# Kernel optimization log

Measured on AMD Instinct MI355X. Metric: run time of the kernel, lower is better.

Reference implementation:

```python
import jax, jax.numpy as jnp
import numpy as np

B, S, H, NH = 2, 2048, 1024, 16
P = H // NH

def setup_inputs() -> dict:
    key = jax.random.key(0)
    k1, k2, k3, k4 = jax.random.split(key, 4)
    x = jax.random.normal(k1, (B, S, H), dtype=jnp.float32)
    mask = jax.random.randint(k2, (B, S), 0, 2).astype(jnp.int32)
    # weights: (num_heads, 3, hidden, partial) -- the leading singleton dim of the
    # torch parameter is pure broadcast, dropped here.
    W = jax.random.normal(k3, (NH, 3, H, P), dtype=jnp.float32) * (1.0 / np.sqrt(H))
    Wl = jax.random.normal(k4, (H, H), dtype=jnp.float32) * (1.0 / np.sqrt(H))
    bl = jnp.zeros((H,), dtype=jnp.float32)
    return {"x": x, "mask": mask, "W": W, "Wl": Wl, "bl": bl}

def reference(x, mask, W, Wl, bl):
    nh, _, h, p = W.shape
    scale = 1.0 / np.sqrt(p)
    # kvq[b, t, n, s, p]; t=0 keys, t=1 values, t=2 queries (unbind order in source)
    kvq = jnp.einsum('bsh,nthp->btnsp', x, W)
    keys, values, queries = kvq[:, 0], kvq[:, 1], kvq[:, 2]  # each [B, NH, S, P]
    # NOTE: source computes keys @ queries^T -> scores[b,n,i,j] = k_i . q_j
    scores = jnp.einsum('bnip,bnjp->bnij', keys, queries) * scale
    # mask==0 zeroes out the LAST axis (query positions), exactly as the fancy-index write
    scores = jnp.where(mask[:, None, None, :] == 0, jnp.float32(-1e12), scores)
    # softmax over dim=2 (key axis), as in the source (Softmax(dim=2))
    w = jax.nn.softmax(scores, axis=2)
    out = jnp.einsum('bnij,bnjp->bnip', w, values)  # [B, NH, S, P]
    b, _, s, _ = out.shape
    hidden = out.transpose(0, 2, 1, 3).reshape(b, s, nh * p)  # concat heads
    return hidden @ Wl.T + bl
```

## Files before the change

### kernel.cpp

```cpp
#include <hip/hip_runtime.h>

#define B_ 2
#define S_ 2048
#define H_ 1024
#define NH_ 16
#define P_ 64

using f32x4 = __attribute__((ext_vector_type(4))) float;
using i32x4 = __attribute__((ext_vector_type(4))) int;
using f16   = _Float16;
using f16x8 = __attribute__((ext_vector_type(8))) f16;
using f16x4 = __attribute__((ext_vector_type(4))) f16;
using h16x2 = __attribute__((ext_vector_type(2))) __fp16;

#define QSCALE 0.18033688f

static __device__ __forceinline__ f16x8 ldh8(const f16* p) { return *(const f16x8*)p; }
static __device__ __forceinline__ f32x4 ld4f(const float* p) { return *(const f32x4*)p; }

static __device__ __forceinline__ f32x4 mm16(f16x8 a, f16x8 b, f32x4 c) {
  return __builtin_amdgcn_mfma_f32_16x16x32_f16(a, b, c, 0, 0, 0);
}

__global__ __launch_bounds__(256) void tw_kernel(
    const float* __restrict__ W, f16* __restrict__ WtH)
{
  __shared__ float T[64 * 65];
  const int tid = threadIdx.x;
  const int nt = blockIdx.x >> 4;
  const int h0 = (blockIdx.x & 15) * 64;
  const float* src = W + (size_t)nt * H_ * P_ + (size_t)h0 * P_;
  #pragma unroll
  for (int r = 0; r < 4; ++r) {
    int idx = tid + r * 256;
    int h = idx >> 4, p4 = (idx & 15) << 2;
    f32x4 v = ld4f(src + (size_t)h * P_ + p4);
    #pragma unroll
    for (int i = 0; i < 4; ++i) T[(p4 + i) * 65 + h] = v[i];
  }
  __syncthreads();
  f16* dh = WtH + (size_t)nt * P_ * H_;
  #pragma unroll
  for (int r = 0; r < 4; ++r) {
    int idx = tid + r * 256;
    int p = idx >> 4, h4 = (idx & 15) << 2;
    f16x4 hv;
    #pragma unroll
    for (int i = 0; i < 4; ++i) hv[i] = (f16)T[p * 65 + h4 + i];
    *(f16x4*)(dh + (size_t)p * H_ + h0 + h4) = hv;
  }
}

__global__ __launch_bounds__(256) void swl_kernel(
    const float* __restrict__ Wl, f16* __restrict__ WlH)
{
  int idx = blockIdx.x * 256 + threadIdx.x;
  f32x4 v = ((const f32x4*)Wl)[idx];
  f16x4 h;
  #pragma unroll
  for (int i = 0; i < 4; ++i) h[i] = (f16)v[i];
  ((f16x4*)WlH)[idx] = h;
}

__global__ __launch_bounds__(256) void qkv_kernel(
    const float* __restrict__ x, const f16* __restrict__ WtH,
    f16* __restrict__ Kh, f16* __restrict__ Qh, f16* __restrict__ VTh)
{
  __shared__ f16 xls[2][64 * 64];

  int blk = blockIdx.x;
  const int st = blk & 31; blk >>= 5;
  const int n = blk & 15;
  const int b = blk >> 4;
  const int s0 = st * 64;
  const int tid = threadIdx.x;
  const int w = tid >> 6, lane = tid & 63, q = lane >> 4, fr = lane & 15;
  const int bn = b * NH_ + n;

  const int srow = tid >> 2, scc = tid & 3;
  const float* xsrc = x + ((size_t)b * S_ + s0 + srow) * H_ + 16 * scc;
  const int c0 = ((2 * scc) ^ (srow & 7)) * 8;
  const int c1 = ((2 * scc + 1) ^ (srow & 7)) * 8;

  auto stage = [&](int k0, int bs) {
    f32x4 v0 = ld4f(xsrc + k0),     v1 = ld4f(xsrc + k0 + 4);
    f32x4 v2 = ld4f(xsrc + k0 + 8), v3 = ld4f(xsrc + k0 + 12);
    f16x8 a, b2;
    #pragma unroll
    for (int e = 0; e < 4; ++e) {
      a[e] = (f16)v0[e];  a[e + 4] = (f16)v1[e];
      b2[e] = (f16)v2[e]; b2[e + 4] = (f16)v3[e];
    }
    *(f16x8*)&xls[bs][srow * 64 + c0] = a;
    *(f16x8*)&xls[bs][srow * 64 + c1] = b2;
  };

  const f16* WtK = WtH + ((size_t)(n * 3 + 0) * P_ + 16 * w + fr) * H_ + 8 * q;
  const f16* WtV = WtH + ((size_t)(n * 3 + 1) * P_ + 16 * w + fr) * H_ + 8 * q;
  const f16* WtQ = WtH + ((size_t)(n * 3 + 2) * P_ + 16 * w + fr) * H_ + 8 * q;

  f32x4 accK[4] = {}, accQ[4] = {}, accV[4] = {};

  stage(0, 0);
  for (int step = 0; step < 16; ++step) {
    __syncthreads();
    if (step < 15) stage((step + 1) * 64, (step + 1) & 1);
    const int bs = step & 1;
    const int k0 = step * 64;

    f16x8 xf[4][2];
    #pragma unroll
    for (int ss = 0; ss < 4; ++ss) {
      int row = 16 * ss + fr;
      #pragma unroll
      for (int ks = 0; ks < 2; ++ks) {
        int ch = ((q + 4 * ks) ^ (row & 7)) * 8;
        xf[ss][ks] = *(const f16x8*)&xls[bs][row * 64 + ch];
      }
    }
    f16x8 wk0 = ldh8(WtK + k0), wk1 = ldh8(WtK + k0 + 32);
    f16x8 wq0 = ldh8(WtQ + k0), wq1 = ldh8(WtQ + k0 + 32);
    f16x8 wv0 = ldh8(WtV + k0), wv1 = ldh8(WtV + k0 + 32);
    #pragma unroll
    for (int ss = 0; ss < 4; ++ss) {
      accK[ss] = mm16(wk0, xf[ss][0], accK[ss]);
      accK[ss] = mm16(wk1, xf[ss][1], accK[ss]);
      accQ[ss] = mm16(wq0, xf[ss][0], accQ[ss]);
      accQ[ss] = mm16(wq1, xf[ss][1], accQ[ss]);
      accV[ss] = mm16(xf[ss][0], wv0, accV[ss]);
      accV[ss] = mm16(xf[ss][1], wv1, accV[ss]);
    }
  }

  #pragma unroll
  for (int ss = 0; ss < 4; ++ss) {
    f16x4 hK, hQ;
    #pragma unroll
    for (int c = 0; c < 4; ++c) {
      hK[c] = (f16)accK[ss][c];
      hQ[c] = (f16)(accQ[ss][c] * QSCALE);
    }
    size_t off = ((size_t)bn * S_ + (s0 + 16 * ss + fr)) * P_ + 16 * w + 4 * q;
    *(f16x4*)(Kh + off) = hK;
    *(f16x4*)(Qh + off) = hQ;
  }
  #pragma unroll
  for (int ss = 0; ss < 4; ++ss) {
    f16x4 hV;
    #pragma unroll
    for (int c = 0; c < 4; ++c) hV[c] = (f16)accV[ss][c];
    size_t off = ((size_t)bn * P_ + (16 * w + fr)) * S_ + s0 + 16 * ss + 4 * q;
    *(f16x4*)(VTh + off) = hV;
  }
}

__global__ __launch_bounds__(256) void stats_kernel(
    const f16* __restrict__ Kh, const f16* __restrict__ Qh,
    float* __restrict__ csuminv)
{
  __shared__ float zbuf[2 * 128];
  const int tid = threadIdx.x;
  const int bid = blockIdx.x;
  const int j0 = (bid & 15) * 128;
  const int bn = bid >> 4;
  const int w = tid >> 6, lane = tid & 63, q = lane >> 4, fr = lane & 15;
  const int jb = 64 * (w & 1), ih = w >> 1, ib0 = 32 * ih;

  f16x8 qf[4][2];
  #pragma unroll
  for (int jt = 0; jt < 4; ++jt)
    #pragma unroll
    for (int ks = 0; ks < 2; ++ks)
      qf[jt][ks] = ldh8(Qh + ((size_t)bn * S_ + (j0 + jb + 16 * jt + fr)) * P_ + 8 * q + 32 * ks);

  f32x4 z[4] = {};
  f16x8 kA[2][2], kB[2][2];

  auto loadK = [&](f16x8 (&kf)[2][2], int i0) {
    #pragma unroll
    for (int it = 0; it < 2; ++it)
      #pragma unroll
      for (int ks = 0; ks < 2; ++ks)
        kf[it][ks] = ldh8(Kh + ((size_t)bn * S_ + (i0 + ib0 + 16 * it + fr)) * P_ + 8 * q + 32 * ks);
  };
  auto step = [&](f16x8 (&kf)[2][2]) {
    f32x4 sc[4][2] = {};
    __builtin_amdgcn_s_setprio(1);
    #pragma unroll
    for (int ks = 0; ks < 2; ++ks)
      #pragma unroll
      for (int jt = 0; jt < 4; ++jt)
        #pragma unroll
        for (int it = 0; it < 2; ++it)
          sc[jt][it] = mm16(qf[jt][ks], kf[it][ks], sc[jt][it]);
    __builtin_amdgcn_s_setprio(0);
    #pragma unroll
    for (int jt = 0; jt < 4; ++jt)
      #pragma unroll
      for (int c = 0; c < 4; ++c)
        z[jt][c] += exp2f(sc[jt][0][c]) + exp2f(sc[jt][1][c]);
  };

  loadK(kA, 0);
  for (int i0 = 0; i0 < S_; i0 += 128) {
    loadK(kB, i0 + 64);
    step(kA);
    loadK(kA, (i0 + 128) & (S_ - 1));
    step(kB);
  }

  #pragma unroll
  for (int msk = 1; msk <= 8; msk <<= 1)
    #pragma unroll
    for (int jt = 0; jt < 4; ++jt)
      #pragma unroll
      for (int c = 0; c < 4; ++c)
        z[jt][c] += __shfl_xor(z[jt][c], msk, 64);

  if (fr == 0) {
    #pragma unroll
    for (int jt = 0; jt < 4; ++jt)
      *(f32x4*)&zbuf[ih * 128 + jb + 16 * jt + 4 * q] = z[jt];
  }
  __syncthreads();
  if (tid < 128)
    csuminv[(size_t)bn * S_ + j0 + tid] = 1.0f / (zbuf[tid] + zbuf[128 + tid]);
}

__global__ __launch_bounds__(256) void scale_kernel(
    f16* __restrict__ VT, const float* __restrict__ csuminv,
    const int* __restrict__ mask, float* __restrict__ Cbuf)
{
  const int bid = blockIdx.x;
  const int bn = bid >> 4;
  const int b = bn >> 4;
  const int p = (bid & 15) * 4 + (threadIdx.x >> 6);
  const int lane = threadIdx.x & 63;
  f16* row = VT + ((size_t)bn * P_ + p) * S_;
  const float* zr = csuminv + (size_t)bn * S_;
  const int* mr = mask + (size_t)b * S_;
  float acc = 0.0f;
  #pragma unroll
  for (int k = 0; k < 4; ++k) {
    int s = (lane + 64 * k) * 8;
    f16x8 v = *(const f16x8*)(row + s);
    f32x4 z0 = ld4f(zr + s), z1 = ld4f(zr + s + 4);
    i32x4 m0 = *(const i32x4*)(mr + s), m1 = *(const i32x4*)(mr + s + 4);
    f16x8 o;
    #pragma unroll
    for (int e = 0; e < 4; ++e) {
      float fv = (float)v[e];
      if (m0[e] != 0) o[e] = (f16)(fv * z0[e]);
      else { o[e] = (f16)0.0f; acc += fv; }
      float fv2 = (float)v[e + 4];
      if (m1[e] != 0) o[e + 4] = (f16)(fv2 * z1[e]);
      else { o[e + 4] = (f16)0.0f; acc += fv2; }
    }
    *(f16x8*)(row + s) = o;
  }
  #pragma unroll
  for (int msk = 1; msk <= 32; msk <<= 1) acc += __shfl_xor(acc, msk, 64);
  if (lane == 0) Cbuf[bn * P_ + p] = acc * (1.0f / S_);
}

__global__ __launch_bounds__(256) void av_kernel(
    const f16* __restrict__ Kh, const f16* __restrict__ Qh,
    const f16* __restrict__ VT, const float* __restrict__ Cbuf,
    f16* __restrict__ hidh)
{
  __shared__ __align__(16) char smem[18432];
  const int tid = threadIdx.x;
  const int bid = blockIdx.x;
  const int i0 = (bid & 31) * 64;
  const int bn = bid >> 5;
  const int b = bn >> 4, n = bn & 15;
  const int w = tid >> 6, lane = tid & 63, q = lane >> 4, fr = lane & 15;
  f16* ew = (f16*)smem + w * (64 * 36);

  f16x8 kf[4][2];
  #pragma unroll
  for (int it = 0; it < 4; ++it)
    #pragma unroll
    for (int ks = 0; ks < 2; ++ks)
      kf[it][ks] = ldh8(Kh + ((size_t)bn * S_ + (i0 + 16 * it + fr)) * P_ + 8 * q + 32 * ks);

  const f16* qp  = Qh + ((size_t)bn * S_ + (w * 32 + fr)) * P_ + 8 * q;
  const f16* vp0 = VT + ((size_t)bn * P_ + fr) * S_ + w * 32 + 8 * q;
  const f16* vp1 = vp0 + (size_t)16 * S_;
  const f16* vp2 = vp0 + (size_t)32 * S_;
  const f16* vp3 = vp0 + (size_t)48 * S_;

  f32x4 opv[4][4] = {};

  for (int T = 0; T < 16; ++T) {
    f16x8 aq00 = ldh8(qp);
    f16x8 aq01 = ldh8(qp + 32);
    f16x8 aq10 = ldh8(qp + 1024);
    f16x8 aq11 = ldh8(qp + 1056);
    f16x8 va0 = ldh8(vp0), va1 = ldh8(vp1), va2 = ldh8(vp2), va3 = ldh8(vp3);
    qp += 128 * 64;
    vp0 += 128; vp1 += 128; vp2 += 128; vp3 += 128;

    #pragma unroll
    for (int it = 0; it < 4; ++it) {
      f32x4 s0 = {}, s1 = {};
      s0 = mm16(aq00, kf[it][0], s0);
      s0 = mm16(aq01, kf[it][1], s0);
      s1 = mm16(aq10, kf[it][0], s1);
      s1 = mm16(aq11, kf[it][1], s1);
      union { f16x4 v; h16x2 h[2]; } e0, e1;
      e0.h[0] = __builtin_amdgcn_cvt_pkrtz(exp2f(s0[0]), exp2f(s0[1]));
      e0.h[1] = __builtin_amdgcn_cvt_pkrtz(exp2f(s0[2]), exp2f(s0[3]));
      e1.h[0] = __builtin_amdgcn_cvt_pkrtz(exp2f(s1[0]), exp2f(s1[1]));
      e1.h[1] = __builtin_amdgcn_cvt_pkrtz(exp2f(s1[2]), exp2f(s1[3]));
      *(f16x4*)(ew + (16 * it + fr) * 36 + 4 * q)      = e0.v;
      *(f16x4*)(ew + (16 * it + fr) * 36 + 16 + 4 * q) = e1.v;
    }

    #pragma unroll
    for (int it = 0; it < 4; ++it) {
      f16x8 ef = *(const f16x8*)(ew + (16 * it + fr) * 36 + 8 * q);
      opv[0][it] = mm16(va0, ef, opv[0][it]);
      opv[1][it] = mm16(va1, ef, opv[1][it]);
      opv[2][it] = mm16(va2, ef, opv[2][it]);
      opv[3][it] = mm16(va3, ef, opv[3][it]);
    }
  }

  float* accl = (float*)smem;
  #pragma unroll
  for (int r = 0; r < 4; ++r) {
    __syncthreads();
    if (w == r) {
      #pragma unroll
      for (int it = 0; it < 4; ++it)
        #pragma unroll
        for (int pt = 0; pt < 4; ++pt) {
          float* a = &accl[(16 * it + fr) * 68 + 16 * pt + 4 * q];
          if (r == 0) *(f32x4*)a = opv[pt][it];
          else {
            f32x4 old = *(const f32x4*)a;
            #pragma unroll
            for (int c = 0; c < 4; ++c) old[c] += opv[pt][it][c];
            *(f32x4*)a = old;
          }
        }
    }
  }
  __syncthreads();

  const int ti = tid >> 2;
  const int tp = (tid & 3) << 4;
  const float* cb = Cbuf + bn * P_ + tp;
  f16* dst = hidh + ((size_t)b * S_ + (i0 + ti)) * H_ + n * P_ + tp;
  #pragma unroll
  for (int h = 0; h < 2; ++h) {
    f32x4 a0 = *(const f32x4*)&accl[ti * 68 + tp + 8 * h];
    f32x4 a1 = *(const f32x4*)&accl[ti * 68 + tp + 8 * h + 4];
    f32x4 c0 = ld4f(cb + 8 * h);
    f32x4 c1 = ld4f(cb + 8 * h + 4);
    f16x8 o;
    #pragma unroll
    for (int e = 0; e < 4; ++e) {
      o[e]     = (f16)(a0[e] + c0[e]);
      o[e + 4] = (f16)(a1[e] + c1[e]);
    }
    *(f16x8*)(dst + 8 * h) = o;
  }
}

__global__ __launch_bounds__(256) void final_kernel(
    const f16* __restrict__ hidh, const f16* __restrict__ WlH,
    const float* __restrict__ bl, float* __restrict__ out)
{
  __shared__ f16 hl[2][64 * 64];
  const int tid = threadIdx.x;
  const int ot = blockIdx.x & 15;
  const int rt = blockIdx.x >> 4;
  const int r0 = rt * 64, o0 = ot * 64;
  const int w = tid >> 6, lane = tid & 63, q = lane >> 4, fr = lane & 15;

  const int srow = tid >> 2, scc = tid & 3;
  const f16* hsrc = hidh + (size_t)(r0 + srow) * H_ + 16 * scc;
  const int c0 = ((2 * scc) ^ (srow & 7)) * 8;
  const int c1 = ((2 * scc + 1) ^ (srow & 7)) * 8;

  auto stage = [&](int k0, int bs) {
    f16x8 a = ldh8(hsrc + k0);
    f16x8 b2 = ldh8(hsrc + k0 + 8);
    *(f16x8*)&hl[bs][srow * 64 + c0] = a;
    *(f16x8*)&hl[bs][srow * 64 + c1] = b2;
  };

  const f16* WlA = WlH + ((size_t)(o0 + 16 * w + fr)) * H_ + 8 * q;

  f32x4 acc[4] = {};

  stage(0, 0);
  for (int step = 0; step < 16; ++step) {
    __syncthreads();
    if (step < 15) stage((step + 1) * 64, (step + 1) & 1);
    const int bs = step & 1;
    const int k0 = step * 64;

    f16x8 bh[4][2];
    #pragma unroll
    for (int ss = 0; ss < 4; ++ss) {
      int row = 16 * ss + fr;
      #pragma unroll
      for (int ks = 0; ks < 2; ++ks) {
        int ch = ((q + 4 * ks) ^ (row & 7)) * 8;
        bh[ss][ks] = *(const f16x8*)&hl[bs][row * 64 + ch];
      }
    }
    f16x8 ah0 = ldh8(WlA + k0);
    f16x8 ah1 = ldh8(WlA + k0 + 32);
    #pragma unroll
    for (int ss = 0; ss < 4; ++ss) {
      acc[ss] = mm16(ah0, bh[ss][0], acc[ss]);
      acc[ss] = mm16(ah1, bh[ss][1], acc[ss]);
    }
  }

  const int o = o0 + 16 * w + 4 * q;
  f32x4 bv = ld4f(bl + o);
  #pragma unroll
  for (int ss = 0; ss < 4; ++ss) {
    f32x4 v;
    #pragma unroll
    for (int c = 0; c < 4; ++c) v[c] = acc[ss][c] + bv[c];
    *(f32x4*)(out + (size_t)(r0 + 16 * ss + fr) * H_ + o) = v;
  }
}

extern "C" void kernel_launch(void* const* d_in, const int* in_sizes, int n_in,
                              void* d_out, int out_size, void* d_ws, size_t ws_size,
                              hipStream_t stream) {
  const float* x    = (const float*)d_in[0];
  const int*   mask = (const int*)d_in[1];
  const float* W    = (const float*)d_in[2];
  const float* Wl   = (const float*)d_in[3];
  const float* bl   = (const float*)d_in[4];
  float* out = (float*)d_out;

  const size_t SZ  = (size_t)B_ * NH_ * S_ * P_;
  const size_t SZW = (size_t)NH_ * 3 * H_ * P_;
  const size_t SZL = (size_t)H_ * H_;
  const size_t SZC = (size_t)B_ * NH_ * S_;
  const size_t SZH = (size_t)B_ * S_ * H_;

  char* p = (char*)d_ws;
  f16*   Kh   = (f16*)p;  p += SZ * 2;
  f16*   Qh   = (f16*)p;  p += SZ * 2;
  f16*   VTh  = (f16*)p;  p += SZ * 2;
  f16*   WtH  = (f16*)p;  p += SZW * 2;
  f16*   WlH  = (f16*)p;  p += SZL * 2;
  f16*   hidh = (f16*)p;  p += SZH * 2;
  float* csuminv = (float*)p; p += SZC * 4;
  float* Cbuf    = (float*)p; p += (size_t)B_ * NH_ * P_ * 4;

  tw_kernel   <<<NH_ * 3 * (H_ / 64), 256, 0, stream>>>(W, WtH);
  swl_kernel  <<<(SZL / 4) / 256, 256, 0, stream>>>(Wl, WlH);
  qkv_kernel  <<<B_ * NH_ * (S_ / 64), 256, 0, stream>>>(x, WtH, Kh, Qh, VTh);
  stats_kernel<<<B_ * NH_ * (S_ / 128), 256, 0, stream>>>(Kh, Qh, csuminv);
  scale_kernel<<<B_ * NH_ * 16, 256, 0, stream>>>(VTh, csuminv, mask, Cbuf);
  av_kernel   <<<B_ * NH_ * (S_ / 64), 256, 0, stream>>>(
      Kh, Qh, VTh, Cbuf, hidh);
  final_kernel<<<(B_ * S_ / 64) * (H_ / 64), 256, 0, stream>>>(
      hidh, WlH, bl, out);
}
```

Baseline: 218.6 us.

## Fuse weight prep kernels, fold V scaling into stats, keep exp tiles in registers

Merges the two weight-conversion kernels into one launch and folds the V-column scaling and mask-sum into the stats kernel, reducing Cbuf with atomics after a memset. This removes the csuminv round trip and one launch. In the AV kernel, the exponentiated score fragment now feeds the MFMA straight from registers instead of being staged through LDS. To make that valid, V is loaded as two 4-wide halves arranged to match the MFMA operand layout. The costs are float atomic ordering nondeterminism, an extra memset, and narrower V loads.

```diff
diff --git a/kernel.cpp b/kernel.cpp
--- a/kernel.cpp
+++ b/kernel.cpp
@@ -16,50 +16,50 @@
 #define QSCALE 0.18033688f
 
 static __device__ __forceinline__ f16x8 ldh8(const f16* p) { return *(const f16x8*)p; }
+static __device__ __forceinline__ f16x4 ldh4(const f16* p) { return *(const f16x4*)p; }
 static __device__ __forceinline__ f32x4 ld4f(const float* p) { return *(const f32x4*)p; }
 
 static __device__ __forceinline__ f32x4 mm16(f16x8 a, f16x8 b, f32x4 c) {
   return __builtin_amdgcn_mfma_f32_16x16x32_f16(a, b, c, 0, 0, 0);
 }
 
-__global__ __launch_bounds__(256) void tw_kernel(
-    const float* __restrict__ W, f16* __restrict__ WtH)
+__global__ __launch_bounds__(256) void prep_kernel(
+    const float* __restrict__ W, const float* __restrict__ Wl,
+    f16* __restrict__ WtH, f16* __restrict__ WlH)
 {
   __shared__ float T[64 * 65];
   const int tid = threadIdx.x;
-  const int nt = blockIdx.x >> 4;
-  const int h0 = (blockIdx.x & 15) * 64;
-  const float* src = W + (size_t)nt * H_ * P_ + (size_t)h0 * P_;
-  #pragma unroll
-  for (int r = 0; r < 4; ++r) {
-    int idx = tid + r * 256;
-    int h = idx >> 4, p4 = (idx & 15) << 2;
-    f32x4 v = ld4f(src + (size_t)h * P_ + p4);
-    #pragma unroll
-    for (int i = 0; i < 4; ++i) T[(p4 + i) * 65 + h] = v[i];
-  }
-  __syncthreads();
-  f16* dh = WtH + (size_t)nt * P_ * H_;
-  #pragma unroll
-  for (int r = 0; r < 4; ++r) {
-    int idx = tid + r * 256;
-    int p = idx >> 4, h4 = (idx & 15) << 2;
-    f16x4 hv;
-    #pragma unroll
-    for (int i = 0; i < 4; ++i) hv[i] = (f16)T[p * 65 + h4 + i];
-    *(f16x4*)(dh + (size_t)p * H_ + h0 + h4) = hv;
-  }
-}
-
-__global__ __launch_bounds__(256) void swl_kernel(
-    const float* __restrict__ Wl, f16* __restrict__ WlH)
-{
-  int idx = blockIdx.x * 256 + threadIdx.x;
-  f32x4 v = ((const f32x4*)Wl)[idx];
-  f16x4 h;
-  #pragma unroll
-  for (int i = 0; i < 4; ++i) h[i] = (f16)v[i];
-  ((f16x4*)WlH)[idx] = h;
+  if (blockIdx.x < 768) {
+    const int nt = blockIdx.x >> 4;
+    const int h0 = (blockIdx.x & 15) * 64;
+    const float* src = W + (size_t)nt * H_ * P_ + (size_t)h0 * P_;
+    #pragma unroll
+    for (int r = 0; r < 4; ++r) {
+      int idx = tid + r * 256;
+      int h = idx >> 4, p4 = (idx & 15) << 2;
+      f32x4 v = ld4f(src + (size_t)h * P_ + p4);
+      #pragma unroll
+      for (int i = 0; i < 4; ++i) T[(p4 + i) * 65 + h] = v[i];
+    }
+    __syncthreads();
+    f16* dh = WtH + (size_t)nt * P_ * H_;
+    #pragma unroll
+    for (int r = 0; r < 4; ++r) {
+      int idx = tid + r * 256;
+      int p = idx >> 4, h4 = (idx & 15) << 2;
+      f16x4 hv;
+      #pragma unroll
+      for (int i = 0; i < 4; ++i) hv[i] = (f16)T[p * 65 + h4 + i];
+      *(f16x4*)(dh + (size_t)p * H_ + h0 + h4) = hv;
+    }
+  } else {
+    int idx = (blockIdx.x - 768) * 256 + tid;
+    f32x4 v = ((const f32x4*)Wl)[idx];
+    f16x4 h;
+    #pragma unroll
+    for (int i = 0; i < 4; ++i) h[i] = (f16)v[i];
+    ((f16x4*)WlH)[idx] = h;
+  }
 }
 
 __global__ __launch_bounds__(256) void qkv_kernel(
@@ -156,7 +156,8 @@
 
 __global__ __launch_bounds__(256) void stats_kernel(
     const f16* __restrict__ Kh, const f16* __restrict__ Qh,
-    float* __restrict__ csuminv)
+    f16* __restrict__ VT, const int* __restrict__ mask,
+    float* __restrict__ Cbuf)
 {
   __shared__ float zbuf[2 * 128];
   const int tid = threadIdx.x;
@@ -224,43 +225,29 @@
   }
   __syncthreads();
   if (tid < 128)
-    csuminv[(size_t)bn * S_ + j0 + tid] = 1.0f / (zbuf[tid] + zbuf[128 + tid]);
-}
-
-__global__ __launch_bounds__(256) void scale_kernel(
-    f16* __restrict__ VT, const float* __restrict__ csuminv,
-    const int* __restrict__ mask, float* __restrict__ Cbuf)
-{
-  const int bid = blockIdx.x;
-  const int bn = bid >> 4;
-  const int b = bn >> 4;
-  const int p = (bid & 15) * 4 + (threadIdx.x >> 6);
-  const int lane = threadIdx.x & 63;
-  f16* row = VT + ((size_t)bn * P_ + p) * S_;
-  const float* zr = csuminv + (size_t)bn * S_;
-  const int* mr = mask + (size_t)b * S_;
+    zbuf[tid] = 1.0f / (zbuf[tid] + zbuf[128 + tid]);
+  __syncthreads();
+
+  const int sp = tid >> 2;
+  const int jc = (tid & 3) * 32;
+  f16* vrow = VT + ((size_t)bn * P_ + sp) * S_ + j0 + jc;
+  const int* mr = mask + (size_t)(bn >> 4) * S_ + j0 + jc;
   float acc = 0.0f;
   #pragma unroll
   for (int k = 0; k < 4; ++k) {
-    int s = (lane + 64 * k) * 8;
-    f16x8 v = *(const f16x8*)(row + s);
-    f32x4 z0 = ld4f(zr + s), z1 = ld4f(zr + s + 4);
-    i32x4 m0 = *(const i32x4*)(mr + s), m1 = *(const i32x4*)(mr + s + 4);
+    f16x8 v = *(const f16x8*)(vrow + 8 * k);
     f16x8 o;
     #pragma unroll
-    for (int e = 0; e < 4; ++e) {
+    for (int e = 0; e < 8; ++e) {
       float fv = (float)v[e];
-      if (m0[e] != 0) o[e] = (f16)(fv * z0[e]);
+      if (mr[8 * k + e] != 0) o[e] = (f16)(fv * zbuf[jc + 8 * k + e]);
       else { o[e] = (f16)0.0f; acc += fv; }
-      float fv2 = (float)v[e + 4];
-      if (m1[e] != 0) o[e + 4] = (f16)(fv2 * z1[e]);
-      else { o[e + 4] = (f16)0.0f; acc += fv2; }
-    }
-    *(f16x8*)(row + s) = o;
-  }
-  #pragma unroll
-  for (int msk = 1; msk <= 32; msk <<= 1) acc += __shfl_xor(acc, msk, 64);
-  if (lane == 0) Cbuf[bn * P_ + p] = acc * (1.0f / S_);
+    }
+    *(f16x8*)(vrow + 8 * k) = o;
+  }
+  acc += __shfl_xor(acc, 1, 64);
+  acc += __shfl_xor(acc, 2, 64);
+  if ((tid & 3) == 0) atomicAdd(&Cbuf[bn * P_ + sp], acc * (1.0f / S_));
 }
 
 __global__ __launch_bounds__(256) void av_kernel(
@@ -268,14 +255,13 @@
     const f16* __restrict__ VT, const float* __restrict__ Cbuf,
     f16* __restrict__ hidh)
 {
-  __shared__ __align__(16) char smem[18432];
+  __shared__ __align__(16) float accl[64 * 68];
   const int tid = threadIdx.x;
   const int bid = blockIdx.x;
   const int i0 = (bid & 31) * 64;
   const int bn = bid >> 5;
   const int b = bn >> 4, n = bn & 15;
   const int w = tid >> 6, lane = tid & 63, q = lane >> 4, fr = lane & 15;
-  f16* ew = (f16*)smem + w * (64 * 36);
 
   f16x8 kf[4][2];
   #pragma unroll
@@ -284,11 +270,8 @@
     for (int ks = 0; ks < 2; ++ks)
       kf[it][ks] = ldh8(Kh + ((size_t)bn * S_ + (i0 + 16 * it + fr)) * P_ + 8 * q + 32 * ks);
 
-  const f16* qp  = Qh + ((size_t)bn * S_ + (w * 32 + fr)) * P_ + 8 * q;
-  const f16* vp0 = VT + ((size_t)bn * P_ + fr) * S_ + w * 32 + 8 * q;
-  const f16* vp1 = vp0 + (size_t)16 * S_;
-  const f16* vp2 = vp0 + (size_t)32 * S_;
-  const f16* vp3 = vp0 + (size_t)48 * S_;
+  const f16* qp = Qh + ((size_t)bn * S_ + (w * 32 + fr)) * P_ + 8 * q;
+  const f16* vp = VT + ((size_t)bn * P_ + fr) * S_ + w * 32 + 4 * q;
 
   f32x4 opv[4][4] = {};
 
@@ -297,9 +280,16 @@
     f16x8 aq01 = ldh8(qp + 32);
     f16x8 aq10 = ldh8(qp + 1024);
     f16x8 aq11 = ldh8(qp + 1056);
-    f16x8 va0 = ldh8(vp0), va1 = ldh8(vp1), va2 = ldh8(vp2), va3 = ldh8(vp3);
+    f16x8 va[4];
+    #pragma unroll
+    for (int pt = 0; pt < 4; ++pt) {
+      union { f16x8 v8; f16x4 h4[2]; } u;
+      u.h4[0] = ldh4(vp + (size_t)(16 * pt) * S_);
+      u.h4[1] = ldh4(vp + (size_t)(16 * pt) * S_ + 16);
+      va[pt] = u.v8;
+    }
     qp += 128 * 64;
-    vp0 += 128; vp1 += 128; vp2 += 128; vp3 += 128;
+    vp += 128;
 
     #pragma unroll
     for (int it = 0; it < 4; ++it) {
@@ -308,26 +298,18 @@
       s0 = mm16(aq01, kf[it][1], s0);
       s1 = mm16(aq10, kf[it][0], s1);
       s1 = mm16(aq11, kf[it][1], s1);
-      union { f16x4 v; h16x2 h[2]; } e0, e1;
-      e0.h[0] = __builtin_amdgcn_cvt_pkrtz(exp2f(s0[0]), exp2f(s0[1]));
-      e0.h[1] = __builtin_amdgcn_cvt_pkrtz(exp2f(s0[2]), exp2f(s0[3]));
-      e1.h[0] = __builtin_amdgcn_cvt_pkrtz(exp2f(s1[0]), exp2f(s1[1]));
-      e1.h[1] = __builtin_amdgcn_cvt_pkrtz(exp2f(s1[2]), exp2f(s1[3]));
-      *(f16x4*)(ew + (16 * it + fr) * 36 + 4 * q)      = e0.v;
-      *(f16x4*)(ew + (16 * it + fr) * 36 + 16 + 4 * q) = e1.v;
-    }
-
-    #pragma unroll
-    for (int it = 0; it < 4; ++it) {
-      f16x8 ef = *(const f16x8*)(ew + (16 * it + fr) * 36 + 8 * q);
-      opv[0][it] = mm16(va0, ef, opv[0][it]);
-      opv[1][it] = mm16(va1, ef, opv[1][it]);
-      opv[2][it] = mm16(va2, ef, opv[2][it]);
-      opv[3][it] = mm16(va3, ef, opv[3][it]);
-    }
-  }
-
-  float* accl = (float*)smem;
+      union { f16x8 v8; h16x2 h[4]; } ef;
+      ef.h[0] = __builtin_amdgcn_cvt_pkrtz(exp2f(s0[0]), exp2f(s0[1]));
+      ef.h[1] = __builtin_amdgcn_cvt_pkrtz(exp2f(s0[2]), exp2f(s0[3]));
+      ef.h[2] = __builtin_amdgcn_cvt_pkrtz(exp2f(s1[0]), exp2f(s1[1]));
+      ef.h[3] = __builtin_amdgcn_cvt_pkrtz(exp2f(s1[2]), exp2f(s1[3]));
+      opv[0][it] = mm16(va[0], ef.v8, opv[0][it]);
+      opv[1][it] = mm16(va[1], ef.v8, opv[1][it]);
+      opv[2][it] = mm16(va[2], ef.v8, opv[2][it]);
+      opv[3][it] = mm16(va[3], ef.v8, opv[3][it]);
+    }
+  }
+
   #pragma unroll
   for (int r = 0; r < 4; ++r) {
     __syncthreads();
@@ -446,7 +428,6 @@
   const size_t SZ  = (size_t)B_ * NH_ * S_ * P_;
   const size_t SZW = (size_t)NH_ * 3 * H_ * P_;
   const size_t SZL = (size_t)H_ * H_;
-  const size_t SZC = (size_t)B_ * NH_ * S_;
   const size_t SZH = (size_t)B_ * S_ * H_;
 
   char* p = (char*)d_ws;
@@ -456,14 +437,13 @@
   f16*   WtH  = (f16*)p;  p += SZW * 2;
   f16*   WlH  = (f16*)p;  p += SZL * 2;
   f16*   hidh = (f16*)p;  p += SZH * 2;
-  float* csuminv = (float*)p; p += SZC * 4;
-  float* Cbuf    = (float*)p; p += (size_t)B_ * NH_ * P_ * 4;
-
-  tw_kernel   <<<NH_ * 3 * (H_ / 64), 256, 0, stream>>>(W, WtH);
-  swl_kernel  <<<(SZL / 4) / 256, 256, 0, stream>>>(Wl, WlH);
+  float* Cbuf = (float*)p; p += (size_t)B_ * NH_ * P_ * 4;
+
+  prep_kernel <<<1792, 256, 0, stream>>>(W, Wl, WtH, WlH);
   qkv_kernel  <<<B_ * NH_ * (S_ / 64), 256, 0, stream>>>(x, WtH, Kh, Qh, VTh);
-  stats_kernel<<<B_ * NH_ * (S_ / 128), 256, 0, stream>>>(Kh, Qh, csuminv);
-  scale_kernel<<<B_ * NH_ * 16, 256, 0, stream>>>(VTh, csuminv, mask, Cbuf);
+  hipMemsetAsync(Cbuf, 0, (size_t)B_ * NH_ * P_ * 4, stream);
+  stats_kernel<<<B_ * NH_ * (S_ / 128), 256, 0, stream>>>(
+      Kh, Qh, VTh, mask, Cbuf);
   av_kernel   <<<B_ * NH_ * (S_ / 64), 256, 0, stream>>>(
       Kh, Qh, VTh, Cbuf, hidh);
   final_kernel<<<(B_ * S_ / 64) * (H_ / 64), 256, 0, stream>>>(
```

New measurement: 241.3 us. +10.4%, slower.
